# Performance work log

Hardware: AMD Instinct MI355X
Metric: run time of the kernel (lower is better)

## Reference

```python
import jax, jax.numpy as jnp
import numpy as np
import math

K = 7
PAD = 3

def _aniso_kernel(k, sigma_h, sigma_v, angle):
    ax = np.linspace(-(k // 2), k // 2, k, dtype=np.float32)
    xx, yy = np.meshgrid(ax, ax, indexing='ij')
    x_rot = xx * math.cos(angle) + yy * math.sin(angle)
    y_rot = -xx * math.sin(angle) + yy * math.cos(angle)
    ker = np.exp(-(x_rot ** 2 / (2 * sigma_h ** 2) + y_rot ** 2 / (2 * sigma_v ** 2)))
    ker = ker / (ker.sum() + 1e-8)
    return jnp.asarray(ker, dtype=jnp.float32)  # (k,k)

BASE_H = _aniso_kernel(K, 2.5, 1.0, 0.0)
BASE_V = _aniso_kernel(K, 2.5, 1.0, math.pi / 2)

def setup_inputs() -> dict:
    key = jax.random.key(0)
    k1, k2, k3, k4 = jax.random.split(key, 4)
    B, C, H, W, MID = 8, 256, 128, 128, 16
    x = jax.random.normal(k1, (B, C, H, W), dtype=jnp.float32)
    angle_map = jax.random.uniform(k2, (B, H, W), dtype=jnp.float32) * math.pi
    w_reduce = jax.random.normal(k3, (MID, C), dtype=jnp.float32) * 0.05
    w_expand = jax.random.normal(k4, (C, MID), dtype=jnp.float32) * 0.05
    return {"x": x, "angle_map": angle_map, "w_reduce": w_reduce, "w_expand": w_expand}

def reference(x, angle_map, w_reduce, w_expand):
    B, C, H, W = x.shape
    # 1x1 conv reduce: (B,C,H,W) x (mid,C) -> (B,mid,H,W)
    x_low = jnp.einsum('bchw,mc->bmhw', x, w_reduce)
    # per-pixel blend weights
    w_h = jnp.cos(angle_map) ** 2                      # (B,H,W)
    combined = (w_h[..., None, None] * BASE_H
                + (1.0 - w_h)[..., None, None] * BASE_V)  # (B,H,W,k,k)
    combined = combined.reshape(B, H, W, K * K)
    # reflect pad and extract kxk patches (stride 1 -> output spatial == H,W)
    x_pad = jnp.pad(x_low, ((0, 0), (0, 0), (PAD, PAD), (PAD, PAD)), mode='reflect')
    patches = jnp.stack(
        [x_pad[:, :, i:i + H, j:j + W] for i in range(K) for j in range(K)],
        axis=-1)                                       # (B,mid,H,W,k*k)
    out_low = jnp.einsum('bmhwk,bhwk->bmhw', patches, combined)
    out_low = jnp.nan_to_num(out_low)
    out = jnp.einsum('bmhw,cm->bchw', out_low, w_expand)
    return jnp.nan_to_num(out)
```

## Files before the change

kernel.cpp:

```cpp
#include <hip/hip_runtime.h>

#define Bn   8
#define Cn   256
#define MIDn 16
#define Hn   128
#define Wn   128
#define HWn  (Hn * Wn)

__global__ __launch_bounds__(256, 4) void reduce_k(const float2* __restrict__ x2,
                                                   const float* __restrict__ wr,
                                                   float2* __restrict__ xlow2) {
    __shared__ float2 comb[4][MIDn][64];

    const int tid = threadIdx.x;
    const int p2  = tid & 63;
    const int wv  = tid >> 6;
    const int b   = blockIdx.y;
    const int p0  = blockIdx.x * 64;

    const int c0 = __builtin_amdgcn_readfirstlane(wv << 6);

    const float2* xb = x2 + ((size_t)b * Cn + c0) * (HWn / 2) + p0 + p2;

    float2 acc[MIDn];
#pragma unroll
    for (int m = 0; m < MIDn; ++m) acc[m] = make_float2(0.f, 0.f);

#pragma unroll 8
    for (int c = 0; c < 64; ++c) {
        const float2 v = xb[(size_t)c * (HWn / 2)];
        const float* w = wr + (c0 + c);
#pragma unroll
        for (int m = 0; m < MIDn; ++m) {
            const float wm = w[m * Cn];
            acc[m].x = fmaf(v.x, wm, acc[m].x);
            acc[m].y = fmaf(v.y, wm, acc[m].y);
        }
    }

#pragma unroll
    for (int m = 0; m < MIDn; ++m) comb[wv][m][p2] = acc[m];
    __syncthreads();

    float2* ob = xlow2 + (size_t)b * MIDn * (HWn / 2) + p0;
#pragma unroll
    for (int k = 0; k < 4; ++k) {
        const int idx = k * 256 + tid;
        const int m   = idx >> 6;
        const int q   = idx & 63;
        const float2 s0 = comb[0][m][q];
        const float2 s1 = comb[1][m][q];
        const float2 s2 = comb[2][m][q];
        const float2 s3 = comb[3][m][q];
        float2 s;
        s.x = (s0.x + s1.x) + (s2.x + s3.x);
        s.y = (s0.y + s1.y) + (s2.y + s3.y);
        ob[(size_t)m * (HWn / 2) + q] = s;
    }
}

#define TW 32
#define TH 8
#define HR (TH + 6)
#define WR (TW + 6)

__device__ __forceinline__ int reflect_i(int i, int n) {
    return i < 0 ? -i : (i >= n ? 2 * n - 2 - i : i);
}

__global__ __launch_bounds__(256, 2) void conv_expand_k(const float* __restrict__ xlow,
                                                        const float* __restrict__ ang,
                                                        const float* __restrict__ we,
                                                        float* __restrict__ out) {
    __shared__ float tile[MIDn][HR][WR];

    const int tid = threadIdx.x;
    const int b   = blockIdx.y;
    const int rem = blockIdx.x;
    const int th0 = (rem >> 2) * TH;
    const int tw0 = (rem & 3) * TW;

    const float* pb = xlow + (size_t)b * MIDn * HWn;
    for (int idx = tid; idx < MIDn * HR * WR; idx += 256) {
        const int m  = idx / (HR * WR);
        const int r2 = idx - m * (HR * WR);
        const int r  = r2 / WR;
        const int cc = r2 - r * WR;
        const int gr = reflect_i(th0 + r - 3, Hn);
        const int gc = reflect_i(tw0 + cc - 3, Wn);
        tile[m][r][cc] = pb[(size_t)m * HWn + gr * Wn + gc];
    }
    __syncthreads();

    const int pc = tid & (TW - 1);
    const int pr = tid >> 5;
    const int gh = th0 + pr;
    const int gw = tw0 + pc;

    const float a  = ang[(size_t)b * HWn + gh * Wn + gw];
    const float ch = cosf(a);
    const float wh = ch * ch;

    const float fu[7] = {0.48675226f, 0.72614904f, 0.92311635f, 1.0f,
                         0.92311635f, 0.72614904f, 0.48675226f};
    const float fv[7] = {0.011108997f, 0.13533528f, 0.60653066f, 1.0f,
                         0.60653066f, 0.13533528f, 0.011108997f};
    const float su = 1.f + 2.f * (0.48675226f + 0.72614904f + 0.92311635f);
    const float sv = 1.f + 2.f * (0.011108997f + 0.13533528f + 0.60653066f);
    const float inv = 1.f / (su * sv + 1e-8f);
    const float aH = wh * inv;
    const float aV = (1.f - wh) * inv;

    float wcomb[49];
#pragma unroll
    for (int i = 0; i < 7; ++i)
#pragma unroll
        for (int j = 0; j < 7; ++j)
            wcomb[i * 7 + j] = aH * (fu[i] * fv[j]) + aV * (fv[i] * fu[j]);

    float low[MIDn];
#pragma unroll
    for (int m = 0; m < MIDn; ++m) {
        float acc = 0.f;
#pragma unroll
        for (int i = 0; i < 7; ++i)
#pragma unroll
            for (int j = 0; j < 7; ++j)
                acc = fmaf(wcomb[i * 7 + j], tile[m][pr + i][pc + j], acc);
        low[m] = acc;
    }

    float* ob = out + (size_t)b * Cn * HWn + gh * Wn + gw;
#pragma unroll 4
    for (int c = 0; c < Cn; ++c) {
        const float* w = we + (size_t)c * MIDn;
        float o = 0.f;
#pragma unroll
        for (int m = 0; m < MIDn; ++m) o = fmaf(w[m], low[m], o);
        ob[(size_t)c * HWn] = o;
    }
}

extern "C" void kernel_launch(void* const* d_in, const int* in_sizes, int n_in,
                              void* d_out, int out_size, void* d_ws, size_t ws_size,
                              hipStream_t stream) {
    const float* x   = (const float*)d_in[0];
    const float* ang = (const float*)d_in[1];
    const float* wr  = (const float*)d_in[2];
    const float* we  = (const float*)d_in[3];
    float*       out = (float*)d_out;

    float* xlow = (float*)d_ws;

    reduce_k<<<dim3((HWn / 2) / 64, Bn), dim3(256), 0, stream>>>(
        (const float2*)x, wr, (float2*)xlow);
    conv_expand_k<<<dim3(64, Bn), dim3(256), 0, stream>>>(xlow, ang, we, out);
}
```

Baseline: 314.7 us.

## Split conv_expand work across channel groups with smaller tiles and float2 stores

Halves the tile height so each block covers 128 pixels, and splits the 7x7 blended conv across two thread halves that each handle 8 of the 16 mid channels, staging the results in shared memory. The expand stage then has each wave produce 64 output channels for 64 pixel pairs, writing float2 stores. Doubling the grid and raising the occupancy hint target better latency hiding and wider stores for the output write, which is the dominant cost. The trade-offs are more halo overlap per tile, an extra barrier, and added shared memory use.

Measured after the change: 258.8 us. -17.8%, faster.

```diff
diff --git a/kernel.cpp b/kernel.cpp
--- a/kernel.cpp
+++ b/kernel.cpp
@@ -60,19 +60,21 @@
 }
 
 #define TW 32
-#define TH 8
+#define TH 4
 #define HR (TH + 6)
 #define WR (TW + 6)
+#define NPX (TH * TW)
 
 __device__ __forceinline__ int reflect_i(int i, int n) {
     return i < 0 ? -i : (i >= n ? 2 * n - 2 - i : i);
 }
 
-__global__ __launch_bounds__(256, 2) void conv_expand_k(const float* __restrict__ xlow,
+__global__ __launch_bounds__(256, 4) void conv_expand_k(const float* __restrict__ xlow,
                                                         const float* __restrict__ ang,
                                                         const float* __restrict__ we,
-                                                        float* __restrict__ out) {
+                                                        float2* __restrict__ out2) {
     __shared__ float tile[MIDn][HR][WR];
+    __shared__ float low[MIDn][NPX];
 
     const int tid = threadIdx.x;
     const int b   = blockIdx.y;
@@ -92,52 +94,69 @@
     }
     __syncthreads();
 
-    const int pc = tid & (TW - 1);
-    const int pr = tid >> 5;
-    const int gh = th0 + pr;
-    const int gw = tw0 + pc;
+    {
+        const int px = tid & (NPX - 1);
+        const int mh = tid >> 7;
+        const int pr = px >> 5;
+        const int pc = px & 31;
 
-    const float a  = ang[(size_t)b * HWn + gh * Wn + gw];
-    const float ch = cosf(a);
-    const float wh = ch * ch;
+        const float a  = ang[(size_t)b * HWn + (th0 + pr) * Wn + (tw0 + pc)];
+        const float ch = cosf(a);
+        const float wh = ch * ch;
 
-    const float fu[7] = {0.48675226f, 0.72614904f, 0.92311635f, 1.0f,
-                         0.92311635f, 0.72614904f, 0.48675226f};
-    const float fv[7] = {0.011108997f, 0.13533528f, 0.60653066f, 1.0f,
-                         0.60653066f, 0.13533528f, 0.011108997f};
-    const float su = 1.f + 2.f * (0.48675226f + 0.72614904f + 0.92311635f);
-    const float sv = 1.f + 2.f * (0.011108997f + 0.13533528f + 0.60653066f);
-    const float inv = 1.f / (su * sv + 1e-8f);
-    const float aH = wh * inv;
-    const float aV = (1.f - wh) * inv;
+        const float fu[7] = {0.48675226f, 0.72614904f, 0.92311635f, 1.0f,
+                             0.92311635f, 0.72614904f, 0.48675226f};
+        const float fv[7] = {0.011108997f, 0.13533528f, 0.60653066f, 1.0f,
+                             0.60653066f, 0.13533528f, 0.011108997f};
+        const float su = 1.f + 2.f * (0.48675226f + 0.72614904f + 0.92311635f);
+        const float sv = 1.f + 2.f * (0.011108997f + 0.13533528f + 0.60653066f);
+        const float inv = 1.f / (su * sv + 1e-8f);
+        const float aH = wh * inv;
+        const float aV = (1.f - wh) * inv;
 
-    float wcomb[49];
-#pragma unroll
-    for (int i = 0; i < 7; ++i)
-#pragma unroll
-        for (int j = 0; j < 7; ++j)
-            wcomb[i * 7 + j] = aH * (fu[i] * fv[j]) + aV * (fv[i] * fu[j]);
-
-    float low[MIDn];
-#pragma unroll
-    for (int m = 0; m < MIDn; ++m) {
-        float acc = 0.f;
+        float wcomb[49];
 #pragma unroll
         for (int i = 0; i < 7; ++i)
 #pragma unroll
             for (int j = 0; j < 7; ++j)
-                acc = fmaf(wcomb[i * 7 + j], tile[m][pr + i][pc + j], acc);
-        low[m] = acc;
+                wcomb[i * 7 + j] = aH * (fu[i] * fv[j]) + aV * (fv[i] * fu[j]);
+
+        const int m0 = mh * 8;
+#pragma unroll
+        for (int mm = 0; mm < 8; ++mm) {
+            float acc = 0.f;
+#pragma unroll
+            for (int i = 0; i < 7; ++i)
+#pragma unroll
+                for (int j = 0; j < 7; ++j)
+                    acc = fmaf(wcomb[i * 7 + j], tile[m0 + mm][pr + i][pc + j], acc);
+            low[m0 + mm][px] = acc;
+        }
     }
+    __syncthreads();
 
-    float* ob = out + (size_t)b * Cn * HWn + gh * Wn + gw;
+    const int p2 = tid & 63;
+    const int c0 = __builtin_amdgcn_readfirstlane((tid >> 6) << 6);
+
+    const float2* low2 = (const float2*)low;
+    float2 lw[MIDn];
+#pragma unroll
+    for (int m = 0; m < MIDn; ++m) lw[m] = low2[m * 64 + p2];
+
+    const int gh  = th0 + (p2 >> 4);
+    const int gw2 = (tw0 >> 1) + (p2 & 15);
+    float2* ob = out2 + ((size_t)b * Cn + c0) * (HWn / 2) + gh * (Wn / 2) + gw2;
+
 #pragma unroll 4
-    for (int c = 0; c < Cn; ++c) {
-        const float* w = we + (size_t)c * MIDn;
-        float o = 0.f;
+    for (int ci = 0; ci < 64; ++ci) {
+        const float* w = we + (size_t)(c0 + ci) * MIDn;
+        float2 o = make_float2(0.f, 0.f);
 #pragma unroll
-        for (int m = 0; m < MIDn; ++m) o = fmaf(w[m], low[m], o);
-        ob[(size_t)c * HWn] = o;
+        for (int m = 0; m < MIDn; ++m) {
+            o.x = fmaf(w[m], lw[m].x, o.x);
+            o.y = fmaf(w[m], lw[m].y, o.y);
+        }
+        ob[(size_t)ci * (HWn / 2)] = o;
     }
 }
 
@@ -154,5 +173,5 @@
 
     reduce_k<<<dim3((HWn / 2) / 64, Bn), dim3(256), 0, stream>>>(
         (const float2*)x, wr, (float2*)xlow);
-    conv_expand_k<<<dim3(64, Bn), dim3(256), 0, stream>>>(xlow, ang, we, out);
+    conv_expand_k<<<dim3(128, Bn), dim3(256), 0, stream>>>(xlow, ang, we, (float2*)out);
 }
```
